# Kernel optimization log

Measured on AMD Instinct MI355X. Metric: run time of the kernel, lower is better.

## Reference

```python
import jax, jax.numpy as jnp
import numpy as np

DIM = 1024
H = 16
DH = DIM // H
THETA = 10000.0


def _rotary_cos_sin(dtype):
    # Faithful to original: rotary is called on q with shape (B, H, 1, DH) and
    # seq_dim=1, so "positions" are t = arange(num_heads).
    inv_freq = 1.0 / (THETA ** (jnp.arange(0, DH, 2, dtype=jnp.float32) / DH))
    t = jnp.arange(H, dtype=jnp.float32)
    freqs = t[:, None] * inv_freq[None, :]          # (H, DH/2)
    emb = jnp.concatenate([freqs, freqs], axis=-1)   # (H, DH)
    cos = jnp.cos(emb)[None, :, None, :].astype(dtype)  # (1, H, 1, DH)
    sin = jnp.sin(emb)[None, :, None, :].astype(dtype)
    return cos, sin


def _rotate_half(x):
    x1, x2 = x[..., : DH // 2], x[..., DH // 2 :]
    return jnp.concatenate([-x2, x1], axis=-1)


def setup_inputs() -> dict:
    key = jax.random.key(0)
    ks = jax.random.split(key, 6)
    B, N = 16, 4096
    s = 1.0 / np.sqrt(DIM)
    return {
        "x": jax.random.normal(ks[0], (B, N, DIM), dtype=jnp.float32),
        "Wq": jax.random.normal(ks[1], (DIM, DIM), dtype=jnp.float32) * s,
        "Wk": jax.random.normal(ks[2], (DIM, DIM), dtype=jnp.float32) * s,
        "Wv": jax.random.normal(ks[3], (DIM, DIM), dtype=jnp.float32) * s,
        "Wp": jax.random.normal(ks[4], (DIM, DIM), dtype=jnp.float32) * s,
        "bp": jax.random.normal(ks[5], (DIM,), dtype=jnp.float32) * 0.01,
    }


def reference(x, Wq, Wk, Wv, Wp, bp):
    B, N, C = x.shape
    scale = DH ** -0.5
    # projections (weights stored as (in, out); x @ W)
    q = (x[:, :1, :] @ Wq).reshape(B, 1, H, DH).transpose(0, 2, 1, 3)  # (B,H,1,DH)
    k = (x @ Wk).reshape(B, N, H, DH).transpose(0, 2, 1, 3)            # (B,H,N,DH)
    v = (x @ Wv).reshape(B, N, H, DH).transpose(0, 2, 1, 3)            # (B,H,N,DH)
    cos, sin = _rotary_cos_sin(x.dtype)
    q = q * cos + _rotate_half(q) * sin
    k = k * cos + _rotate_half(k) * sin  # broadcasts over N (per original)
    attn = jnp.einsum("bhqd,bhkd->bhqk", q, k) * scale  # (B,H,1,N)
    attn = jax.nn.softmax(attn, axis=-1)
    out = jnp.einsum("bhqk,bhkd->bhqd", attn, v)        # (B,H,1,DH)
    out = out.transpose(0, 2, 1, 3).reshape(B, 1, C)
    return out @ Wp + bp
```

## Files before the change

kernel.cpp:

```cpp
#include <hip/hip_runtime.h>

#define NB 16
#define SEQ 4096
#define DIMC 1024
#define NH 16
#define DH 64
#define NC 64
#define RPC 64

#define OFF_Q    0
#define OFF_WTIL 16384
#define OFF_PMAX 278528
#define OFF_LC   294912
#define OFF_HO4  311296
#define OFF_Y    376832

__global__ __launch_bounds__(256) void kq(const float* __restrict__ x,
                                          const float* __restrict__ Wq,
                                          float* __restrict__ qws) {
  const int jc = blockIdx.x, b = blockIdx.y, t = threadIdx.x;
  const int d = t & 63, g = t >> 6;
  const int j = jc * 64 + d;
  const float* x0 = x + (size_t)b * SEQ * DIMC;
  __shared__ float red[256];
  float a = 0.f;
  #pragma unroll 8
  for (int c = g * 256; c < g * 256 + 256; ++c)
    a = fmaf(x0[c], Wq[(size_t)c * DIMC + j], a);
  red[t] = a;
  __syncthreads();
  if (t < 64)
    qws[b * DIMC + jc * 64 + t] = red[t] + red[64 + t] + red[128 + t] + red[192 + t];
}

__global__ __launch_bounds__(256) void kw(const float* __restrict__ Wk,
                                          const float* __restrict__ qws,
                                          float* __restrict__ wtil) {
  const int cb = blockIdx.x, b = blockIdx.y, t = threadIdx.x;
  const int w = t >> 6, l = t & 63;
  float4 qreg[4];
  {
    const float4* q4 = (const float4*)(qws + b * DIMC + l * 16);
    #pragma unroll
    for (int i = 0; i < 4; ++i) qreg[i] = q4[i];
  }
  const int h = l >> 2;
  float* wt = wtil + ((size_t)b * NH + h) * DIMC;
  #pragma unroll 4
  for (int i = 0; i < 16; ++i) {
    const int c = cb * 64 + w * 16 + i;
    const float4* row = (const float4*)(Wk + (size_t)c * DIMC) + l * 4;
    float s = 0.f;
    #pragma unroll
    for (int k = 0; k < 4; ++k) {
      float4 rv = row[k];
      s = fmaf(rv.x, qreg[k].x, s); s = fmaf(rv.y, qreg[k].y, s);
      s = fmaf(rv.z, qreg[k].z, s); s = fmaf(rv.w, qreg[k].w, s);
    }
    s += __shfl_xor(s, 1);
    s += __shfl_xor(s, 2);
    if ((l & 3) == 0) wt[c] = s * 0.125f;
  }
}

__device__ __forceinline__ float dot16(const float4* xv, const float4* wv) {
  float s = 0.f;
  #pragma unroll
  for (int i = 0; i < 4; ++i) {
    s = fmaf(xv[i].x, wv[i].x, s); s = fmaf(xv[i].y, wv[i].y, s);
    s = fmaf(xv[i].z, wv[i].z, s); s = fmaf(xv[i].w, wv[i].w, s);
  }
  return s;
}

__global__ __launch_bounds__(256) void k_la(const float* __restrict__ x,
                                            const float* __restrict__ wtil,
                                            float* __restrict__ y,
                                            float* __restrict__ pmax,
                                            float* __restrict__ Lc) {
  const int nc = blockIdx.x, b = blockIdx.y, t = threadIdx.x;
  const int w = t >> 6, l = t & 63;
  __shared__ float4 pl[RPC][4];

  const float4* wt4 = (const float4*)wtil + ((size_t)b * NH + w * 4) * 256;
  float4 wv[4][4];
  #pragma unroll
  for (int h = 0; h < 4; ++h)
    #pragma unroll
    for (int i = 0; i < 4; ++i) wv[h][i] = wt4[h * 256 + i * 64 + l];
  const float4* x4 = (const float4*)x + ((size_t)b * SEQ + nc * RPC) * 256;
  float4 va = make_float4(0.f, 0.f, 0.f, 0.f);

  for (int r = 0; r < RPC; r += 2) {
    float4 xa[4], xb[4];
    #pragma unroll
    for (int i = 0; i < 4; ++i) xa[i] = x4[r * 256 + i * 64 + l];
    #pragma unroll
    for (int i = 0; i < 4; ++i) xb[i] = x4[(r + 1) * 256 + i * 64 + l];
    float4 sa, sb;
    sa.x = dot16(xa, wv[0]); sa.y = dot16(xa, wv[1]);
    sa.z = dot16(xa, wv[2]); sa.w = dot16(xa, wv[3]);
    sb.x = dot16(xb, wv[0]); sb.y = dot16(xb, wv[1]);
    sb.z = dot16(xb, wv[2]); sb.w = dot16(xb, wv[3]);
    #pragma unroll
    for (int o = 1; o < 64; o <<= 1) {
      sa.x += __shfl_xor(sa.x, o); sa.y += __shfl_xor(sa.y, o);
      sa.z += __shfl_xor(sa.z, o); sa.w += __shfl_xor(sa.w, o);
      sb.x += __shfl_xor(sb.x, o); sb.y += __shfl_xor(sb.y, o);
      sb.z += __shfl_xor(sb.z, o); sb.w += __shfl_xor(sb.w, o);
    }
    if (l == r) va = sa;
    if (l == r + 1) va = sb;
  }

  float4 m4 = va;
  #pragma unroll
  for (int o = 1; o < 64; o <<= 1) {
    m4.x = fmaxf(m4.x, __shfl_xor(m4.x, o)); m4.y = fmaxf(m4.y, __shfl_xor(m4.y, o));
    m4.z = fmaxf(m4.z, __shfl_xor(m4.z, o)); m4.w = fmaxf(m4.w, __shfl_xor(m4.w, o));
  }
  float4 pv;
  pv.x = __expf(va.x - m4.x); pv.y = __expf(va.y - m4.y);
  pv.z = __expf(va.z - m4.z); pv.w = __expf(va.w - m4.w);
  float4 s4 = pv;
  #pragma unroll
  for (int o = 1; o < 64; o <<= 1) {
    s4.x += __shfl_xor(s4.x, o); s4.y += __shfl_xor(s4.y, o);
    s4.z += __shfl_xor(s4.z, o); s4.w += __shfl_xor(s4.w, o);
  }
  pl[l][w] = pv;
  if (l == 0) {
    ((float4*)(pmax + ((size_t)b * NC + nc) * NH))[w] = m4;
    ((float4*)(Lc + ((size_t)b * NC + nc) * NH))[w] = s4;
  }
  __syncthreads();

  float4 acc[16];
  #pragma unroll
  for (int h = 0; h < 16; ++h) acc[h] = make_float4(0.f, 0.f, 0.f, 0.f);
  for (int r = 0; r < RPC; r += 2) {
    float4 a0 = pl[r][0], a1 = pl[r][1], a2 = pl[r][2], a3 = pl[r][3];
    float4 b0 = pl[r + 1][0], b1 = pl[r + 1][1], b2 = pl[r + 1][2], b3 = pl[r + 1][3];
    float4 xva = x4[r * 256 + t];
    float4 xvb = x4[(r + 1) * 256 + t];
    #define ACC(h, ev, xv) acc[h].x = fmaf(ev, xv.x, acc[h].x); acc[h].y = fmaf(ev, xv.y, acc[h].y); \
                           acc[h].z = fmaf(ev, xv.z, acc[h].z); acc[h].w = fmaf(ev, xv.w, acc[h].w)
    ACC(0, a0.x, xva); ACC(1, a0.y, xva); ACC(2, a0.z, xva); ACC(3, a0.w, xva);
    ACC(4, a1.x, xva); ACC(5, a1.y, xva); ACC(6, a1.z, xva); ACC(7, a1.w, xva);
    ACC(8, a2.x, xva); ACC(9, a2.y, xva); ACC(10, a2.z, xva); ACC(11, a2.w, xva);
    ACC(12, a3.x, xva); ACC(13, a3.y, xva); ACC(14, a3.z, xva); ACC(15, a3.w, xva);
    ACC(0, b0.x, xvb); ACC(1, b0.y, xvb); ACC(2, b0.z, xvb); ACC(3, b0.w, xvb);
    ACC(4, b1.x, xvb); ACC(5, b1.y, xvb); ACC(6, b1.z, xvb); ACC(7, b1.w, xvb);
    ACC(8, b2.x, xvb); ACC(9, b2.y, xvb); ACC(10, b2.z, xvb); ACC(11, b2.w, xvb);
    ACC(12, b3.x, xvb); ACC(13, b3.y, xvb); ACC(14, b3.z, xvb); ACC(15, b3.w, xvb);
    #undef ACC
  }
  float4* y4 = (float4*)y + (((size_t)b * NC + nc) * NH) * 256;
  #pragma unroll
  for (int h = 0; h < 16; ++h) y4[h * 256 + t] = acc[h];
}

__global__ __launch_bounds__(256) void k_comb(const float* __restrict__ y,
                                              const float* __restrict__ pmax,
                                              const float* __restrict__ Lc,
                                              const float* __restrict__ Wv,
                                              float* __restrict__ ho4) {
  const int cs = blockIdx.x, h = blockIdx.y, b = blockIdx.z, t = threadIdx.x;
  __shared__ float sc[NC];
  __shared__ float ylds[256];
  __shared__ float red[256];
  if (t < 64) {
    float mt = pmax[((size_t)b * NC + t) * NH + h];
    float lt = Lc[((size_t)b * NC + t) * NH + h];
    float M = mt;
    #pragma unroll
    for (int o = 1; o < 64; o <<= 1) M = fmaxf(M, __shfl_xor(M, o));
    float e = __expf(mt - M);
    float L = lt * e;
    #pragma unroll
    for (int o = 1; o < 64; o <<= 1) L += __shfl_xor(L, o);
    sc[t] = e / L;
  }
  __syncthreads();
  const int c = cs * 256 + t;
  float ysum = 0.f;
  #pragma unroll 8
  for (int s = 0; s < NC; ++s)
    ysum = fmaf(y[(((size_t)b * NC + s) * NH + h) * DIMC + c], sc[s], ysum);
  ylds[t] = ysum;
  __syncthreads();
  const int d = t & 63, g = t >> 6;
  float part = 0.f;
  #pragma unroll 4
  for (int k = 0; k < 64; ++k)
    part = fmaf(ylds[g * 64 + k],
                Wv[(size_t)(cs * 256 + g * 64 + k) * DIMC + h * DH + d], part);
  red[t] = part;
  __syncthreads();
  if (t < 64)
    ho4[((size_t)cs * NB + b) * DIMC + h * DH + t] =
        red[t] + red[64 + t] + red[128 + t] + red[192 + t];
}

__global__ __launch_bounds__(256) void k_out(const float* __restrict__ ho4,
                                             const float* __restrict__ Wp,
                                             const float* __restrict__ bp,
                                             float* __restrict__ out) {
  const int jc = blockIdx.x, b = blockIdx.y, t = threadIdx.x;
  __shared__ float hs[1024];
  __shared__ float red[256];
  for (int i = t; i < 1024; i += 256)
    hs[i] = ho4[(size_t)b * DIMC + i] + ho4[(size_t)(NB + b) * DIMC + i] +
            ho4[(size_t)(2 * NB + b) * DIMC + i] + ho4[(size_t)(3 * NB + b) * DIMC + i];
  __syncthreads();
  const int d = t & 63, g = t >> 6;
  const int j = jc * 64 + d;
  float a = 0.f;
  #pragma unroll 8
  for (int i = g * 256; i < g * 256 + 256; ++i)
    a = fmaf(hs[i], Wp[(size_t)i * DIMC + j], a);
  red[t] = a;
  __syncthreads();
  if (t < 64)
    out[(size_t)b * DIMC + jc * 64 + t] =
        red[t] + red[64 + t] + red[128 + t] + red[192 + t] + bp[jc * 64 + t];
}

extern "C" void kernel_launch(void* const* d_in, const int* in_sizes, int n_in,
                              void* d_out, int out_size, void* d_ws, size_t ws_size,
                              hipStream_t stream) {
  const float* x  = (const float*)d_in[0];
  const float* Wq = (const float*)d_in[1];
  const float* Wk = (const float*)d_in[2];
  const float* Wv = (const float*)d_in[3];
  const float* Wp = (const float*)d_in[4];
  const float* bp = (const float*)d_in[5];
  float* out = (float*)d_out;
  float* ws = (float*)d_ws;

  float* qws  = ws + OFF_Q;
  float* wtil = ws + OFF_WTIL;
  float* pmax = ws + OFF_PMAX;
  float* Lc   = ws + OFF_LC;
  float* ho4  = ws + OFF_HO4;
  float* y    = ws + OFF_Y;

  kq<<<dim3(16, NB), 256, 0, stream>>>(x, Wq, qws);
  kw<<<dim3(16, NB), 256, 0, stream>>>(Wk, qws, wtil);
  k_la<<<dim3(NC, NB), 256, 0, stream>>>(x, wtil, y, pmax, Lc);
  k_comb<<<dim3(4, NH, NB), 256, 0, stream>>>(y, pmax, Lc, Wv, ho4);
  k_out<<<dim3(16, NB), 256, 0, stream>>>(ho4, Wp, bp, out);
}
```

Measured before the change: 506.2 us.

## Split score and weighted-sum passes, accumulate across chunks to shrink partial outputs

The fused score+softmax+weighted-x kernel is split in two. The first kernel computes scores with each thread owning a row and writes unnormalized exp values plus per-chunk max and sum. The second kernel applies the global softmax rescale per chunk and accumulates four chunks per block, so only 16 partial y tensors per batch are written instead of 64. The Wv projection kernel is restructured to sum these partials directly, with no cross-slice ho4 reduction. This trades a second full read of x and an extra launch for less partial-sum traffic and a score loop without shuffle reductions.

```diff
diff --git a/kernel.cpp b/kernel.cpp
--- a/kernel.cpp
+++ b/kernel.cpp
@@ -6,14 +6,15 @@
 #define NH 16
 #define DH 64
 #define NC 64
-#define RPC 64
+#define RS 16
 
 #define OFF_Q    0
 #define OFF_WTIL 16384
 #define OFF_PMAX 278528
 #define OFF_LC   294912
-#define OFF_HO4  311296
-#define OFF_Y    376832
+#define OFF_E    311296
+#define OFF_YOUT 1359872
+#define OFF_HO   5554176
 
 __global__ __launch_bounds__(256) void kq(const float* __restrict__ x,
                                           const float* __restrict__ Wq,
@@ -63,54 +64,50 @@
   }
 }
 
-__device__ __forceinline__ float dot16(const float4* xv, const float4* wv) {
-  float s = 0.f;
-  #pragma unroll
-  for (int i = 0; i < 4; ++i) {
-    s = fmaf(xv[i].x, wv[i].x, s); s = fmaf(xv[i].y, wv[i].y, s);
-    s = fmaf(xv[i].z, wv[i].z, s); s = fmaf(xv[i].w, wv[i].w, s);
-  }
-  return s;
-}
-
-__global__ __launch_bounds__(256) void k_la(const float* __restrict__ x,
-                                            const float* __restrict__ wtil,
-                                            float* __restrict__ y,
-                                            float* __restrict__ pmax,
-                                            float* __restrict__ Lc) {
+__global__ __launch_bounds__(256) void kS(const float* __restrict__ x,
+                                          const float* __restrict__ wtil,
+                                          float* __restrict__ e,
+                                          float* __restrict__ pmax,
+                                          float* __restrict__ Lc) {
   const int nc = blockIdx.x, b = blockIdx.y, t = threadIdx.x;
   const int w = t >> 6, l = t & 63;
-  __shared__ float4 pl[RPC][4];
-
-  const float4* wt4 = (const float4*)wtil + ((size_t)b * NH + w * 4) * 256;
-  float4 wv[4][4];
-  #pragma unroll
-  for (int h = 0; h < 4; ++h)
-    #pragma unroll
-    for (int i = 0; i < 4; ++i) wv[h][i] = wt4[h * 256 + i * 64 + l];
-  const float4* x4 = (const float4*)x + ((size_t)b * SEQ + nc * RPC) * 256;
-  float4 va = make_float4(0.f, 0.f, 0.f, 0.f);
-
-  for (int r = 0; r < RPC; r += 2) {
-    float4 xa[4], xb[4];
-    #pragma unroll
-    for (int i = 0; i < 4; ++i) xa[i] = x4[r * 256 + i * 64 + l];
-    #pragma unroll
-    for (int i = 0; i < 4; ++i) xb[i] = x4[(r + 1) * 256 + i * 64 + l];
-    float4 sa, sb;
-    sa.x = dot16(xa, wv[0]); sa.y = dot16(xa, wv[1]);
-    sa.z = dot16(xa, wv[2]); sa.w = dot16(xa, wv[3]);
-    sb.x = dot16(xb, wv[0]); sb.y = dot16(xb, wv[1]);
-    sb.z = dot16(xb, wv[2]); sb.w = dot16(xb, wv[3]);
-    #pragma unroll
-    for (int o = 1; o < 64; o <<= 1) {
-      sa.x += __shfl_xor(sa.x, o); sa.y += __shfl_xor(sa.y, o);
-      sa.z += __shfl_xor(sa.z, o); sa.w += __shfl_xor(sa.w, o);
-      sb.x += __shfl_xor(sb.x, o); sb.y += __shfl_xor(sb.y, o);
-      sb.z += __shfl_xor(sb.z, o); sb.w += __shfl_xor(sb.w, o);
-    }
-    if (l == r) va = sa;
-    if (l == r + 1) va = sb;
+  const int wq = __builtin_amdgcn_readfirstlane(w);
+
+  const float4* xrow = (const float4*)x + ((size_t)b * SEQ + nc * 64 + l) * 256 + wq * 64;
+  const float4* wt   = (const float4*)wtil + ((size_t)b * NH) * 256 + wq * 64;
+
+  float acc[16] = {0.f, 0.f, 0.f, 0.f, 0.f, 0.f, 0.f, 0.f,
+                   0.f, 0.f, 0.f, 0.f, 0.f, 0.f, 0.f, 0.f};
+  for (int k4 = 0; k4 < 64; k4 += 4) {
+    float4 xv[4];
+    #pragma unroll
+    for (int i = 0; i < 4; ++i) xv[i] = xrow[k4 + i];
+    #pragma unroll
+    for (int h = 0; h < 16; ++h) {
+      #pragma unroll
+      for (int i = 0; i < 4; ++i) {
+        float4 wv = wt[h * 256 + k4 + i];
+        acc[h] = fmaf(xv[i].x, wv.x, acc[h]);
+        acc[h] = fmaf(xv[i].y, wv.y, acc[h]);
+        acc[h] = fmaf(xv[i].z, wv.z, acc[h]);
+        acc[h] = fmaf(xv[i].w, wv.w, acc[h]);
+      }
+    }
+  }
+
+  __shared__ float4 part[4][4][64];
+  #pragma unroll
+  for (int q = 0; q < 4; ++q)
+    part[q][w][l] = make_float4(acc[4 * q], acc[4 * q + 1], acc[4 * q + 2], acc[4 * q + 3]);
+  __syncthreads();
+
+  float4 va;
+  {
+    float4 p0 = part[w][0][l], p1 = part[w][1][l], p2 = part[w][2][l], p3 = part[w][3][l];
+    va.x = (p0.x + p1.x) + (p2.x + p3.x);
+    va.y = (p0.y + p1.y) + (p2.y + p3.y);
+    va.z = (p0.z + p1.z) + (p2.z + p3.z);
+    va.w = (p0.w + p1.w) + (p2.w + p3.w);
   }
 
   float4 m4 = va;
@@ -128,81 +125,118 @@
     s4.x += __shfl_xor(s4.x, o); s4.y += __shfl_xor(s4.y, o);
     s4.z += __shfl_xor(s4.z, o); s4.w += __shfl_xor(s4.w, o);
   }
-  pl[l][w] = pv;
+  ((float4*)e)[((size_t)b * SEQ + nc * 64 + l) * 4 + w] = pv;
   if (l == 0) {
     ((float4*)(pmax + ((size_t)b * NC + nc) * NH))[w] = m4;
     ((float4*)(Lc + ((size_t)b * NC + nc) * NH))[w] = s4;
   }
-  __syncthreads();
+}
+
+__global__ __launch_bounds__(256) void kY(const float* __restrict__ x,
+                                          const float* __restrict__ e,
+                                          const float* __restrict__ pmax,
+                                          const float* __restrict__ Lc,
+                                          float* __restrict__ yout) {
+  const int rs = blockIdx.x, b = blockIdx.y, t = threadIdx.x;
+  __shared__ float4 sc4[NC][4];
+  __shared__ float4 pl[64][4];
+
+  if (t < 64) {
+    const int ch = t;
+    float scl[16];
+    #pragma unroll
+    for (int h = 0; h < 16; ++h) {
+      float m  = pmax[((size_t)b * NC + ch) * NH + h];
+      float lc = Lc[((size_t)b * NC + ch) * NH + h];
+      float M = m;
+      #pragma unroll
+      for (int o = 1; o < 64; o <<= 1) M = fmaxf(M, __shfl_xor(M, o));
+      float ex = __expf(m - M);
+      float lw = lc * ex;
+      #pragma unroll
+      for (int o = 1; o < 64; o <<= 1) lw += __shfl_xor(lw, o);
+      scl[h] = ex / lw;
+    }
+    #pragma unroll
+    for (int q = 0; q < 4; ++q)
+      sc4[ch][q] = make_float4(scl[4 * q], scl[4 * q + 1], scl[4 * q + 2], scl[4 * q + 3]);
+  }
+
+  const float4* x4 = (const float4*)x + (size_t)b * SEQ * 256;
+  const float4* e4 = (const float4*)e + (size_t)b * SEQ * 4;
 
   float4 acc[16];
   #pragma unroll
   for (int h = 0; h < 16; ++h) acc[h] = make_float4(0.f, 0.f, 0.f, 0.f);
-  for (int r = 0; r < RPC; r += 2) {
-    float4 a0 = pl[r][0], a1 = pl[r][1], a2 = pl[r][2], a3 = pl[r][3];
-    float4 b0 = pl[r + 1][0], b1 = pl[r + 1][1], b2 = pl[r + 1][2], b3 = pl[r + 1][3];
-    float4 xva = x4[r * 256 + t];
-    float4 xvb = x4[(r + 1) * 256 + t];
-    #define ACC(h, ev, xv) acc[h].x = fmaf(ev, xv.x, acc[h].x); acc[h].y = fmaf(ev, xv.y, acc[h].y); \
-                           acc[h].z = fmaf(ev, xv.z, acc[h].z); acc[h].w = fmaf(ev, xv.w, acc[h].w)
-    ACC(0, a0.x, xva); ACC(1, a0.y, xva); ACC(2, a0.z, xva); ACC(3, a0.w, xva);
-    ACC(4, a1.x, xva); ACC(5, a1.y, xva); ACC(6, a1.z, xva); ACC(7, a1.w, xva);
-    ACC(8, a2.x, xva); ACC(9, a2.y, xva); ACC(10, a2.z, xva); ACC(11, a2.w, xva);
-    ACC(12, a3.x, xva); ACC(13, a3.y, xva); ACC(14, a3.z, xva); ACC(15, a3.w, xva);
-    ACC(0, b0.x, xvb); ACC(1, b0.y, xvb); ACC(2, b0.z, xvb); ACC(3, b0.w, xvb);
-    ACC(4, b1.x, xvb); ACC(5, b1.y, xvb); ACC(6, b1.z, xvb); ACC(7, b1.w, xvb);
-    ACC(8, b2.x, xvb); ACC(9, b2.y, xvb); ACC(10, b2.z, xvb); ACC(11, b2.w, xvb);
-    ACC(12, b3.x, xvb); ACC(13, b3.y, xvb); ACC(14, b3.z, xvb); ACC(15, b3.w, xvb);
-    #undef ACC
-  }
-  float4* y4 = (float4*)y + (((size_t)b * NC + nc) * NH) * 256;
-  #pragma unroll
-  for (int h = 0; h < 16; ++h) y4[h * 256 + t] = acc[h];
-}
-
-__global__ __launch_bounds__(256) void k_comb(const float* __restrict__ y,
-                                              const float* __restrict__ pmax,
-                                              const float* __restrict__ Lc,
-                                              const float* __restrict__ Wv,
-                                              float* __restrict__ ho4) {
-  const int cs = blockIdx.x, h = blockIdx.y, b = blockIdx.z, t = threadIdx.x;
-  __shared__ float sc[NC];
-  __shared__ float ylds[256];
+
+  for (int c4 = 0; c4 < 4; ++c4) {
+    const int ch = rs * 4 + c4;
+    __syncthreads();
+    {
+      const int r = t >> 2, qd = t & 3;
+      float4 ev = e4[(size_t)(ch * 64 + r) * 4 + qd];
+      float4 s  = sc4[ch][qd];
+      pl[r][qd] = make_float4(ev.x * s.x, ev.y * s.y, ev.z * s.z, ev.w * s.w);
+    }
+    __syncthreads();
+
+    const float4* xc = x4 + (size_t)(ch * 64) * 256;
+    for (int r = 0; r < 64; r += 2) {
+      float4 xva = xc[(size_t)r * 256 + t];
+      float4 xvb = xc[(size_t)(r + 1) * 256 + t];
+      float4 a0 = pl[r][0], a1 = pl[r][1], a2 = pl[r][2], a3 = pl[r][3];
+      float4 b0 = pl[r + 1][0], b1 = pl[r + 1][1], b2 = pl[r + 1][2], b3 = pl[r + 1][3];
+      #define ACC(h, ev, xv) acc[h].x = fmaf(ev, xv.x, acc[h].x); acc[h].y = fmaf(ev, xv.y, acc[h].y); \
+                             acc[h].z = fmaf(ev, xv.z, acc[h].z); acc[h].w = fmaf(ev, xv.w, acc[h].w)
+      ACC(0, a0.x, xva); ACC(1, a0.y, xva); ACC(2, a0.z, xva); ACC(3, a0.w, xva);
+      ACC(4, a1.x, xva); ACC(5, a1.y, xva); ACC(6, a1.z, xva); ACC(7, a1.w, xva);
+      ACC(8, a2.x, xva); ACC(9, a2.y, xva); ACC(10, a2.z, xva); ACC(11, a2.w, xva);
+      ACC(12, a3.x, xva); ACC(13, a3.y, xva); ACC(14, a3.z, xva); ACC(15, a3.w, xva);
+      ACC(0, b0.x, xvb); ACC(1, b0.y, xvb); ACC(2, b0.z, xvb); ACC(3, b0.w, xvb);
+      ACC(4, b1.x, xvb); ACC(5, b1.y, xvb); ACC(6, b1.z, xvb); ACC(7, b1.w, xvb);
+      ACC(8, b2.x, xvb); ACC(9, b2.y, xvb); ACC(10, b2.z, xvb); ACC(11, b2.w, xvb);
+      ACC(12, b3.x, xvb); ACC(13, b3.y, xvb); ACC(14, b3.z, xvb); ACC(15, b3.w, xvb);
+      #undef ACC
+    }
+  }
+
+  float4* yo = (float4*)yout + (((size_t)b * RS + rs) * NH) * 256 + t;
+  #pragma unroll
+  for (int h = 0; h < 16; ++h) yo[h * 256] = acc[h];
+}
+
+__global__ __launch_bounds__(256) void kV(const float* __restrict__ yout,
+                                          const float* __restrict__ Wv,
+                                          float* __restrict__ ho) {
+  const int cq = blockIdx.x, h = blockIdx.y, b = blockIdx.z, t = threadIdx.x;
+  __shared__ float ysum[DIMC];
   __shared__ float red[256];
-  if (t < 64) {
-    float mt = pmax[((size_t)b * NC + t) * NH + h];
-    float lt = Lc[((size_t)b * NC + t) * NH + h];
-    float M = mt;
-    #pragma unroll
-    for (int o = 1; o < 64; o <<= 1) M = fmaxf(M, __shfl_xor(M, o));
-    float e = __expf(mt - M);
-    float L = lt * e;
-    #pragma unroll
-    for (int o = 1; o < 64; o <<= 1) L += __shfl_xor(L, o);
-    sc[t] = e / L;
-  }
-  __syncthreads();
-  const int c = cs * 256 + t;
-  float ysum = 0.f;
+  #pragma unroll
+  for (int i = 0; i < 4; ++i) {
+    const int c = i * 256 + t;
+    float s = 0.f;
+    #pragma unroll
+    for (int r = 0; r < RS; ++r)
+      s += yout[(((size_t)b * RS + r) * NH + h) * DIMC + c];
+    ysum[c] = s;
+  }
+  __syncthreads();
+  const int d = t & 15, g = t >> 4;
+  float a = 0.f;
   #pragma unroll 8
-  for (int s = 0; s < NC; ++s)
-    ysum = fmaf(y[(((size_t)b * NC + s) * NH + h) * DIMC + c], sc[s], ysum);
-  ylds[t] = ysum;
-  __syncthreads();
-  const int d = t & 63, g = t >> 6;
-  float part = 0.f;
-  #pragma unroll 4
-  for (int k = 0; k < 64; ++k)
-    part = fmaf(ylds[g * 64 + k],
-                Wv[(size_t)(cs * 256 + g * 64 + k) * DIMC + h * DH + d], part);
-  red[t] = part;
-  __syncthreads();
-  if (t < 64)
-    ho4[((size_t)cs * NB + b) * DIMC + h * DH + t] =
-        red[t] + red[64 + t] + red[128 + t] + red[192 + t];
-}
-
-__global__ __launch_bounds__(256) void k_out(const float* __restrict__ ho4,
+  for (int i = 0; i < 64; ++i)
+    a = fmaf(ysum[g * 64 + i], Wv[(size_t)(g * 64 + i) * DIMC + h * DH + cq * 16 + d], a);
+  red[t] = a;
+  __syncthreads();
+  if (t < 16) {
+    float s = 0.f;
+    #pragma unroll
+    for (int j = 0; j < 16; ++j) s += red[j * 16 + t];
+    ho[(size_t)b * DIMC + h * DH + cq * 16 + t] = s;
+  }
+}
+
+__global__ __launch_bounds__(256) void k_out(const float* __restrict__ ho,
                                              const float* __restrict__ Wp,
                                              const float* __restrict__ bp,
                                              float* __restrict__ out) {
@@ -210,8 +244,7 @@
   __shared__ float hs[1024];
   __shared__ float red[256];
   for (int i = t; i < 1024; i += 256)
-    hs[i] = ho4[(size_t)b * DIMC + i] + ho4[(size_t)(NB + b) * DIMC + i] +
-            ho4[(size_t)(2 * NB + b) * DIMC + i] + ho4[(size_t)(3 * NB + b) * DIMC + i];
+    hs[i] = ho[(size_t)b * DIMC + i];
   __syncthreads();
   const int d = t & 63, g = t >> 6;
   const int j = jc * 64 + d;
@@ -242,12 +275,14 @@
   float* wtil = ws + OFF_WTIL;
   float* pmax = ws + OFF_PMAX;
   float* Lc   = ws + OFF_LC;
-  float* ho4  = ws + OFF_HO4;
-  float* y    = ws + OFF_Y;
+  float* e    = ws + OFF_E;
+  float* yout = ws + OFF_YOUT;
+  float* ho   = ws + OFF_HO;
 
   kq<<<dim3(16, NB), 256, 0, stream>>>(x, Wq, qws);
   kw<<<dim3(16, NB), 256, 0, stream>>>(Wk, qws, wtil);
-  k_la<<<dim3(NC, NB), 256, 0, stream>>>(x, wtil, y, pmax, Lc);
-  k_comb<<<dim3(4, NH, NB), 256, 0, stream>>>(y, pmax, Lc, Wv, ho4);
-  k_out<<<dim3(16, NB), 256, 0, stream>>>(ho4, Wp, bp, out);
-}
+  kS<<<dim3(NC, NB), 256, 0, stream>>>(x, wtil, e, pmax, Lc);
+  kY<<<dim3(RS, NB), 256, 0, stream>>>(x, e, pmax, Lc, yout);
+  kV<<<dim3(4, NH, NB), 256, 0, stream>>>(yout, Wv, ho);
+  k_out<<<dim3(16, NB), 256, 0, stream>>>(ho, Wp, bp, out);
+}
```

Result: slower. 561.0 us (+10.8%).

## Stage x tiles in LDS with online softmax to avoid reloading x

Applied to the files above, without the earlier changes.

The main attention kernel now processes its 64 rows in four groups of 16. Each x row is loaded from global memory once, used for the logit dot products, and kept in shared memory for the weighted accumulation pass, so x is no longer read a second time. A running max and rescaling (online softmax) keeps the per-group results exact. The change adds 64KB of LDS, extra barriers and rescale work, and a launch-bounds hint of 2 blocks per CU that may limit occupancy.

```diff
diff --git a/kernel.cpp b/kernel.cpp
--- a/kernel.cpp
+++ b/kernel.cpp
@@ -6,7 +6,6 @@
 #define NH 16
 #define DH 64
 #define NC 64
-#define RPC 64
 
 #define OFF_Q    0
 #define OFF_WTIL 16384
@@ -73,14 +72,16 @@
   return s;
 }
 
-__global__ __launch_bounds__(256) void k_la(const float* __restrict__ x,
-                                            const float* __restrict__ wtil,
-                                            float* __restrict__ y,
-                                            float* __restrict__ pmax,
-                                            float* __restrict__ Lc) {
+__global__ __launch_bounds__(256, 2) void kF(const float* __restrict__ x,
+                                             const float* __restrict__ wtil,
+                                             float* __restrict__ y,
+                                             float* __restrict__ pmax,
+                                             float* __restrict__ Lc) {
   const int nc = blockIdx.x, b = blockIdx.y, t = threadIdx.x;
   const int w = t >> 6, l = t & 63;
-  __shared__ float4 pl[RPC][4];
+  __shared__ float4 xt[16][256];
+  __shared__ float4 pl[16][4];
+  __shared__ float4 esl[4];
 
   const float4* wt4 = (const float4*)wtil + ((size_t)b * NH + w * 4) * 256;
   float4 wv[4][4];
@@ -88,76 +89,104 @@
   for (int h = 0; h < 4; ++h)
     #pragma unroll
     for (int i = 0; i < 4; ++i) wv[h][i] = wt4[h * 256 + i * 64 + l];
-  const float4* x4 = (const float4*)x + ((size_t)b * SEQ + nc * RPC) * 256;
-  float4 va = make_float4(0.f, 0.f, 0.f, 0.f);
-
-  for (int r = 0; r < RPC; r += 2) {
-    float4 xa[4], xb[4];
-    #pragma unroll
-    for (int i = 0; i < 4; ++i) xa[i] = x4[r * 256 + i * 64 + l];
-    #pragma unroll
-    for (int i = 0; i < 4; ++i) xb[i] = x4[(r + 1) * 256 + i * 64 + l];
-    float4 sa, sb;
-    sa.x = dot16(xa, wv[0]); sa.y = dot16(xa, wv[1]);
-    sa.z = dot16(xa, wv[2]); sa.w = dot16(xa, wv[3]);
-    sb.x = dot16(xb, wv[0]); sb.y = dot16(xb, wv[1]);
-    sb.z = dot16(xb, wv[2]); sb.w = dot16(xb, wv[3]);
+
+  const float4* x4 = (const float4*)x + ((size_t)b * SEQ + nc * 64) * 256;
+
+  float4 acc[16];
+  #pragma unroll
+  for (int h = 0; h < 16; ++h) acc[h] = make_float4(0.f, 0.f, 0.f, 0.f);
+  const float NEG = -1.0e30f;
+  float4 m_run = make_float4(NEG, NEG, NEG, NEG);
+  float4 l_run = make_float4(0.f, 0.f, 0.f, 0.f);
+
+  for (int g = 0; g < 4; ++g) {
+    float4 va = make_float4(NEG, NEG, NEG, NEG);
+    float4 gm = make_float4(NEG, NEG, NEG, NEG);
+    __syncthreads();
+    for (int j = 0; j < 16; j += 2) {
+      const int r = g * 16 + j;
+      float4 xa[4], xb[4];
+      #pragma unroll
+      for (int i = 0; i < 4; ++i) xa[i] = x4[(size_t)r * 256 + i * 64 + l];
+      #pragma unroll
+      for (int i = 0; i < 4; ++i) xb[i] = x4[(size_t)(r + 1) * 256 + i * 64 + l];
+      float4 sxa = (w == 0) ? xa[0] : (w == 1) ? xa[1] : (w == 2) ? xa[2] : xa[3];
+      float4 sxb = (w == 0) ? xb[0] : (w == 1) ? xb[1] : (w == 2) ? xb[2] : xb[3];
+      xt[j][w * 64 + l] = sxa;
+      xt[j + 1][w * 64 + l] = sxb;
+      float4 sa, sb;
+      sa.x = dot16(xa, wv[0]); sa.y = dot16(xa, wv[1]);
+      sa.z = dot16(xa, wv[2]); sa.w = dot16(xa, wv[3]);
+      sb.x = dot16(xb, wv[0]); sb.y = dot16(xb, wv[1]);
+      sb.z = dot16(xb, wv[2]); sb.w = dot16(xb, wv[3]);
+      #pragma unroll
+      for (int o = 1; o < 64; o <<= 1) {
+        sa.x += __shfl_xor(sa.x, o); sa.y += __shfl_xor(sa.y, o);
+        sa.z += __shfl_xor(sa.z, o); sa.w += __shfl_xor(sa.w, o);
+        sb.x += __shfl_xor(sb.x, o); sb.y += __shfl_xor(sb.y, o);
+        sb.z += __shfl_xor(sb.z, o); sb.w += __shfl_xor(sb.w, o);
+      }
+      gm.x = fmaxf(gm.x, fmaxf(sa.x, sb.x)); gm.y = fmaxf(gm.y, fmaxf(sa.y, sb.y));
+      gm.z = fmaxf(gm.z, fmaxf(sa.z, sb.z)); gm.w = fmaxf(gm.w, fmaxf(sa.w, sb.w));
+      if (l == j) va = sa;
+      if (l == j + 1) va = sb;
+    }
+    float4 m_new;
+    m_new.x = fmaxf(m_run.x, gm.x); m_new.y = fmaxf(m_run.y, gm.y);
+    m_new.z = fmaxf(m_run.z, gm.z); m_new.w = fmaxf(m_run.w, gm.w);
+    float4 es;
+    es.x = __expf(m_run.x - m_new.x); es.y = __expf(m_run.y - m_new.y);
+    es.z = __expf(m_run.z - m_new.z); es.w = __expf(m_run.w - m_new.w);
+    float4 pv;
+    pv.x = __expf(va.x - m_new.x); pv.y = __expf(va.y - m_new.y);
+    pv.z = __expf(va.z - m_new.z); pv.w = __expf(va.w - m_new.w);
+    float4 gs = pv;
     #pragma unroll
     for (int o = 1; o < 64; o <<= 1) {
-      sa.x += __shfl_xor(sa.x, o); sa.y += __shfl_xor(sa.y, o);
-      sa.z += __shfl_xor(sa.z, o); sa.w += __shfl_xor(sa.w, o);
-      sb.x += __shfl_xor(sb.x, o); sb.y += __shfl_xor(sb.y, o);
-      sb.z += __shfl_xor(sb.z, o); sb.w += __shfl_xor(sb.w, o);
-    }
-    if (l == r) va = sa;
-    if (l == r + 1) va = sb;
-  }
-
-  float4 m4 = va;
-  #pragma unroll
-  for (int o = 1; o < 64; o <<= 1) {
-    m4.x = fmaxf(m4.x, __shfl_xor(m4.x, o)); m4.y = fmaxf(m4.y, __shfl_xor(m4.y, o));
-    m4.z = fmaxf(m4.z, __shfl_xor(m4.z, o)); m4.w = fmaxf(m4.w, __shfl_xor(m4.w, o));
-  }
-  float4 pv;
-  pv.x = __expf(va.x - m4.x); pv.y = __expf(va.y - m4.y);
-  pv.z = __expf(va.z - m4.z); pv.w = __expf(va.w - m4.w);
-  float4 s4 = pv;
-  #pragma unroll
-  for (int o = 1; o < 64; o <<= 1) {
-    s4.x += __shfl_xor(s4.x, o); s4.y += __shfl_xor(s4.y, o);
-    s4.z += __shfl_xor(s4.z, o); s4.w += __shfl_xor(s4.w, o);
-  }
-  pl[l][w] = pv;
+      gs.x += __shfl_xor(gs.x, o); gs.y += __shfl_xor(gs.y, o);
+      gs.z += __shfl_xor(gs.z, o); gs.w += __shfl_xor(gs.w, o);
+    }
+    l_run.x = fmaf(l_run.x, es.x, gs.x); l_run.y = fmaf(l_run.y, es.y, gs.y);
+    l_run.z = fmaf(l_run.z, es.z, gs.z); l_run.w = fmaf(l_run.w, es.w, gs.w);
+    m_run = m_new;
+    if (l < 16) pl[l][w] = pv;
+    if (l == 0) esl[w] = es;
+    __syncthreads();
+    {
+      float4 e0 = esl[0], e1 = esl[1], e2 = esl[2], e3 = esl[3];
+      #define RES(h, s) acc[h].x *= s; acc[h].y *= s; acc[h].z *= s; acc[h].w *= s
+      RES(0, e0.x); RES(1, e0.y); RES(2, e0.z); RES(3, e0.w);
+      RES(4, e1.x); RES(5, e1.y); RES(6, e1.z); RES(7, e1.w);
+      RES(8, e2.x); RES(9, e2.y); RES(10, e2.z); RES(11, e2.w);
+      RES(12, e3.x); RES(13, e3.y); RES(14, e3.z); RES(15, e3.w);
+      #undef RES
+    }
+    for (int j = 0; j < 16; j += 2) {
+      float4 xva = xt[j][t];
+      float4 xvb = xt[j + 1][t];
+      float4 a0 = pl[j][0], a1 = pl[j][1], a2 = pl[j][2], a3 = pl[j][3];
+      float4 b0 = pl[j + 1][0], b1 = pl[j + 1][1], b2 = pl[j + 1][2], b3 = pl[j + 1][3];
+      #define ACC(h, ev, xv) acc[h].x = fmaf(ev, xv.x, acc[h].x); acc[h].y = fmaf(ev, xv.y, acc[h].y); \
+                             acc[h].z = fmaf(ev, xv.z, acc[h].z); acc[h].w = fmaf(ev, xv.w, acc[h].w)
+      ACC(0, a0.x, xva); ACC(1, a0.y, xva); ACC(2, a0.z, xva); ACC(3, a0.w, xva);
+      ACC(4, a1.x, xva); ACC(5, a1.y, xva); ACC(6, a1.z, xva); ACC(7, a1.w, xva);
+      ACC(8, a2.x, xva); ACC(9, a2.y, xva); ACC(10, a2.z, xva); ACC(11, a2.w, xva);
+      ACC(12, a3.x, xva); ACC(13, a3.y, xva); ACC(14, a3.z, xva); ACC(15, a3.w, xva);
+      ACC(0, b0.x, xvb); ACC(1, b0.y, xvb); ACC(2, b0.z, xvb); ACC(3, b0.w, xvb);
+      ACC(4, b1.x, xvb); ACC(5, b1.y, xvb); ACC(6, b1.z, xvb); ACC(7, b1.w, xvb);
+      ACC(8, b2.x, xvb); ACC(9, b2.y, xvb); ACC(10, b2.z, xvb); ACC(11, b2.w, xvb);
+      ACC(12, b3.x, xvb); ACC(13, b3.y, xvb); ACC(14, b3.z, xvb); ACC(15, b3.w, xvb);
+      #undef ACC
+    }
+  }
+
+  float4* y4 = (float4*)y + (((size_t)b * NC + nc) * NH) * 256;
+  #pragma unroll
+  for (int h = 0; h < 16; ++h) y4[h * 256 + t] = acc[h];
   if (l == 0) {
-    ((float4*)(pmax + ((size_t)b * NC + nc) * NH))[w] = m4;
-    ((float4*)(Lc + ((size_t)b * NC + nc) * NH))[w] = s4;
-  }
-  __syncthreads();
-
-  float4 acc[16];
-  #pragma unroll
-  for (int h = 0; h < 16; ++h) acc[h] = make_float4(0.f, 0.f, 0.f, 0.f);
-  for (int r = 0; r < RPC; r += 2) {
-    float4 a0 = pl[r][0], a1 = pl[r][1], a2 = pl[r][2], a3 = pl[r][3];
-    float4 b0 = pl[r + 1][0], b1 = pl[r + 1][1], b2 = pl[r + 1][2], b3 = pl[r + 1][3];
-    float4 xva = x4[r * 256 + t];
-    float4 xvb = x4[(r + 1) * 256 + t];
-    #define ACC(h, ev, xv) acc[h].x = fmaf(ev, xv.x, acc[h].x); acc[h].y = fmaf(ev, xv.y, acc[h].y); \
-                           acc[h].z = fmaf(ev, xv.z, acc[h].z); acc[h].w = fmaf(ev, xv.w, acc[h].w)
-    ACC(0, a0.x, xva); ACC(1, a0.y, xva); ACC(2, a0.z, xva); ACC(3, a0.w, xva);
-    ACC(4, a1.x, xva); ACC(5, a1.y, xva); ACC(6, a1.z, xva); ACC(7, a1.w, xva);
-    ACC(8, a2.x, xva); ACC(9, a2.y, xva); ACC(10, a2.z, xva); ACC(11, a2.w, xva);
-    ACC(12, a3.x, xva); ACC(13, a3.y, xva); ACC(14, a3.z, xva); ACC(15, a3.w, xva);
-    ACC(0, b0.x, xvb); ACC(1, b0.y, xvb); ACC(2, b0.z, xvb); ACC(3, b0.w, xvb);
-    ACC(4, b1.x, xvb); ACC(5, b1.y, xvb); ACC(6, b1.z, xvb); ACC(7, b1.w, xvb);
-    ACC(8, b2.x, xvb); ACC(9, b2.y, xvb); ACC(10, b2.z, xvb); ACC(11, b2.w, xvb);
-    ACC(12, b3.x, xvb); ACC(13, b3.y, xvb); ACC(14, b3.z, xvb); ACC(15, b3.w, xvb);
-    #undef ACC
-  }
-  float4* y4 = (float4*)y + (((size_t)b * NC + nc) * NH) * 256;
-  #pragma unroll
-  for (int h = 0; h < 16; ++h) y4[h * 256 + t] = acc[h];
+    ((float4*)(pmax + ((size_t)b * NC + nc) * NH))[w] = m_run;
+    ((float4*)(Lc + ((size_t)b * NC + nc) * NH))[w] = l_run;
+  }
 }
 
 __global__ __launch_bounds__(256) void k_comb(const float* __restrict__ y,
@@ -247,7 +276,7 @@
 
   kq<<<dim3(16, NB), 256, 0, stream>>>(x, Wq, qws);
   kw<<<dim3(16, NB), 256, 0, stream>>>(Wk, qws, wtil);
-  k_la<<<dim3(NC, NB), 256, 0, stream>>>(x, wtil, y, pmax, Lc);
+  kF<<<dim3(NC, NB), 256, 0, stream>>>(x, wtil, y, pmax, Lc);
   k_comb<<<dim3(4, NH, NB), 256, 0, stream>>>(y, pmax, Lc, Wv, ho4);
   k_out<<<dim3(16, NB), 256, 0, stream>>>(ho4, Wp, bp, out);
 }
```

New measurement: 948.3 us. 1.87x slower.
